# Kernel tuning notes

Measured on AMD Instinct MI355X. Metric: run time of the kernel, lower is better.

## Reference

```python
import jax, jax.numpy as jnp
import numpy as np

NEG_SLOPE = 0.2
EPS = 1e-16


def add_self_loops(edge_index, num_nodes):
    loops = jnp.arange(num_nodes, dtype=edge_index.dtype)
    loops = jnp.stack([loops, loops])  # [2, N]
    return jnp.concatenate([edge_index, loops], axis=1)


def gat_conv(x, edge_index, W, att_src, att_dst, bias, heads, out_c, concat):
    # x: [N, F_in]; edge_index: [2, E] (src row 0 -> dst row 1)
    N = x.shape[0]
    h = (x @ W).reshape(N, heads, out_c)            # [N, H, C]
    src, dst = edge_index[0], edge_index[1]
    a_src = (h * att_src).sum(-1)                    # [N, H]
    a_dst = (h * att_dst).sum(-1)                    # [N, H]
    e = a_src[src] + a_dst[dst]                      # [E, H]
    e = jnp.where(e > 0, e, NEG_SLOPE * e)           # leaky_relu
    # segment softmax over destination node
    m = jax.ops.segment_max(e, dst, num_segments=N)  # [N, H]
    ex = jnp.exp(e - m[dst])                         # [E, H]
    denom = jax.ops.segment_sum(ex, dst, num_segments=N)  # [N, H]
    alpha = ex / (denom[dst] + EPS)                  # [E, H]
    msg = alpha[:, :, None] * h[src]                 # [E, H, C]
    out = jax.ops.segment_sum(msg, dst, num_segments=N)   # [N, H, C]
    if concat:
        out = out.reshape(N, heads * out_c)
    else:
        out = out.mean(axis=1)
    return out + bias


def setup_inputs() -> dict:
    key = jax.random.key(0)
    ks = jax.random.split(key, 12)
    N, E, F_IN, HID, H1, OUT = 100000, 1600000, 512, 8, 8, 40
    x = jax.random.normal(ks[0], (N, F_IN), dtype=jnp.float32)
    edge_index = jax.random.randint(ks[1], (2, E), 0, N, dtype=jnp.int64)
    glorot = lambda k, shp: jax.random.normal(k, shp, jnp.float32) * jnp.sqrt(2.0 / (shp[0] + shp[-1]))
    W1 = glorot(ks[2], (F_IN, H1 * HID))
    att_src1 = glorot(ks[3], (H1, HID))
    att_dst1 = glorot(ks[4], (H1, HID))
    b1 = jnp.zeros((H1 * HID,), jnp.float32)
    W2 = glorot(ks[5], (H1 * HID, 1 * OUT))
    att_src2 = glorot(ks[6], (1, OUT))
    att_dst2 = glorot(ks[7], (1, OUT))
    b2 = jnp.zeros((OUT,), jnp.float32)
    return {"x": x, "edge_index": edge_index, "W1": W1, "att_src1": att_src1,
            "att_dst1": att_dst1, "b1": b1, "W2": W2, "att_src2": att_src2,
            "att_dst2": att_dst2, "b2": b2}


def reference(x, edge_index, W1, att_src1, att_dst1, b1, W2, att_src2, att_dst2, b2):
    N = x.shape[0]
    ei = add_self_loops(edge_index, N)
    h = gat_conv(x, ei, W1, att_src1, att_dst1, b1, heads=8, out_c=8, concat=True)
    h = jax.nn.relu(h)
    # dropout p=0.0 / eval mode -> identity
    out = gat_conv(h, ei, W2, att_src2, att_dst2, b2, heads=1, out_c=40, concat=False)
    return jax.nn.log_softmax(out, axis=1)
```

## Files before the change

### kernel.cpp

```cpp
#include <hip/hip_runtime.h>
#include <math.h>

#define NEG_SLOPE 0.2f
#define EPS_DEN 1e-16f

__device__ __forceinline__ float leaky(float v) { return v > 0.f ? v : NEG_SLOPE * v; }

typedef __attribute__((ext_vector_type(8))) short bf16x8;
typedef __attribute__((ext_vector_type(4))) float f32x4;

__device__ __forceinline__ unsigned bf16rne(float f) {
    unsigned u = __float_as_uint(f);
    return (u + 0x7FFFu + ((u >> 16) & 1u)) >> 16;
}
__device__ __forceinline__ unsigned pack2(float a, float b) {
    return bf16rne(a) | (bf16rne(b) << 16);
}
__device__ __forceinline__ float bfu(unsigned short u) {
    return __uint_as_float(((unsigned)u) << 16);
}

__global__ __launch_bounds__(256) void gemm1_mfma(
    const float* __restrict__ x, const float* __restrict__ W1,
    unsigned short* __restrict__ h1b, int N)
{
    __shared__ __align__(16) unsigned short As[128 * 40];
    __shared__ __align__(16) unsigned short Bs[64 * 40];

    const int t = threadIdx.x;
    const int w = t >> 6;
    const int lane = t & 63;
    const int m16 = lane & 15;
    const int quad = lane >> 4;
    const int rowBase = blockIdx.x * 128;

    f32x4 acc[2][4];
#pragma unroll
    for (int i = 0; i < 2; ++i)
#pragma unroll
        for (int j = 0; j < 4; ++j) acc[i][j] = (f32x4){0.f, 0.f, 0.f, 0.f};

    const float4* x4 = (const float4*)x;

#pragma unroll 1
    for (int chunk = 0; chunk < 16; ++chunk) {
        const int k0 = chunk * 32;
#pragma unroll
        for (int r = 0; r < 4; ++r) {
            int e = t + r * 256;
            int row = e >> 3;
            int kg = e & 7;
            int grow = rowBase + row;
            float4 v = make_float4(0.f, 0.f, 0.f, 0.f);
            if (grow < N) v = x4[(size_t)grow * 128 + (k0 >> 2) + kg];
            uint2 pk = make_uint2(pack2(v.x, v.y), pack2(v.z, v.w));
            *(uint2*)&As[row * 40 + kg * 4] = pk;
        }
        {
            int c = lane;
            int jb = w * 8;
            float f[8];
#pragma unroll
            for (int j = 0; j < 8; ++j) f[j] = W1[(size_t)(k0 + jb + j) * 64 + c];
            uint4 pk;
            pk.x = pack2(f[0], f[1]); pk.y = pack2(f[2], f[3]);
            pk.z = pack2(f[4], f[5]); pk.w = pack2(f[6], f[7]);
            *(uint4*)&Bs[c * 40 + jb] = pk;
        }
        __syncthreads();
        bf16x8 a0 = *(const bf16x8*)&As[(w * 32 + m16) * 40 + quad * 8];
        bf16x8 a1 = *(const bf16x8*)&As[(w * 32 + 16 + m16) * 40 + quad * 8];
#pragma unroll
        for (int j = 0; j < 4; ++j) {
            bf16x8 b = *(const bf16x8*)&Bs[(j * 16 + m16) * 40 + quad * 8];
            acc[0][j] = __builtin_amdgcn_mfma_f32_16x16x32_bf16(a0, b, acc[0][j], 0, 0, 0);
            acc[1][j] = __builtin_amdgcn_mfma_f32_16x16x32_bf16(a1, b, acc[1][j], 0, 0, 0);
        }
        __syncthreads();
    }

#pragma unroll
    for (int i = 0; i < 2; ++i)
#pragma unroll
        for (int reg = 0; reg < 4; ++reg) {
            int r = rowBase + w * 32 + i * 16 + quad * 4 + reg;
            if (r < N) {
#pragma unroll
                for (int j = 0; j < 4; ++j)
                    h1b[(size_t)r * 64 + j * 16 + m16] = (unsigned short)bf16rne(acc[i][j][reg]);
            }
        }
}

__global__ __launch_bounds__(256) void att1_kernel(
    const unsigned short* __restrict__ h1b, const float* __restrict__ att_src,
    const float* __restrict__ att_dst, float* __restrict__ a_src,
    float* __restrict__ a_dst, int N)
{
    int g = blockIdx.x * 256 + threadIdx.x;
    int row = g >> 3, h = g & 7;
    if (row >= N) return;
    uint4 pk = *(const uint4*)(h1b + (size_t)row * 64 + h * 8);
    float v[8];
    v[0] = __uint_as_float(pk.x << 16); v[1] = __uint_as_float(pk.x & 0xFFFF0000u);
    v[2] = __uint_as_float(pk.y << 16); v[3] = __uint_as_float(pk.y & 0xFFFF0000u);
    v[4] = __uint_as_float(pk.z << 16); v[5] = __uint_as_float(pk.z & 0xFFFF0000u);
    v[6] = __uint_as_float(pk.w << 16); v[7] = __uint_as_float(pk.w & 0xFFFF0000u);
    float ps = 0.f, pd = 0.f;
#pragma unroll
    for (int c = 0; c < 8; ++c) {
        ps += v[c] * att_src[h * 8 + c];
        pd += v[c] * att_dst[h * 8 + c];
    }
    a_src[(size_t)row * 8 + h] = ps;
    a_dst[(size_t)row * 8 + h] = pd;
}

__global__ __launch_bounds__(256) void deg_kernel(
    const int* __restrict__ ei, unsigned* __restrict__ deg, int E, int Etot)
{
    int idx = blockIdx.x * blockDim.x + threadIdx.x;
    if (idx >= Etot) return;
    int d = (idx < E) ? ei[E + idx] : (idx - E);
    atomicAdd(&deg[d], 1u);
}

__global__ __launch_bounds__(256) void scanA_kernel(
    const unsigned* __restrict__ deg, unsigned* __restrict__ loc,
    unsigned* __restrict__ bsum, int N)
{
    __shared__ unsigned sh[256];
    int i = blockIdx.x * 256 + threadIdx.x;
    unsigned v = (i < N) ? deg[i] : 0u;
    sh[threadIdx.x] = v;
    __syncthreads();
    for (int off = 1; off < 256; off <<= 1) {
        unsigned u = (threadIdx.x >= (unsigned)off) ? sh[threadIdx.x - off] : 0u;
        __syncthreads();
        sh[threadIdx.x] += u;
        __syncthreads();
    }
    if (i < N) loc[i] = sh[threadIdx.x] - v;
    if (threadIdx.x == 255) bsum[blockIdx.x] = sh[255];
}

__global__ __launch_bounds__(1024) void scanB_kernel(unsigned* __restrict__ bsum, int nb)
{
    __shared__ unsigned sh[1024];
    int t = threadIdx.x;
    unsigned carry = 0;
    for (int base = 0; base < nb; base += 1024) {
        int i = base + t;
        unsigned v = (i < nb) ? bsum[i] : 0u;
        sh[t] = v;
        __syncthreads();
        for (int off = 1; off < 1024; off <<= 1) {
            unsigned u = (t >= off) ? sh[t - off] : 0u;
            __syncthreads();
            sh[t] += u;
            __syncthreads();
        }
        unsigned incl = sh[t];
        unsigned tot  = sh[1023];
        __syncthreads();
        if (i < nb) bsum[i] = incl - v + carry;
        carry += tot;
        __syncthreads();
    }
}

__global__ __launch_bounds__(256) void scanC_kernel(
    const unsigned* __restrict__ loc, const unsigned* __restrict__ bsum,
    unsigned* __restrict__ rowstart, unsigned* __restrict__ cursor, int N, int Etot)
{
    int i = blockIdx.x * 256 + threadIdx.x;
    if (i >= N) return;
    unsigned r = loc[i] + bsum[blockIdx.x];
    rowstart[i] = r;
    cursor[i] = r;
    if (i == 0) rowstart[N] = (unsigned)Etot;
}

__global__ __launch_bounds__(256) void scatter_kernel(
    const int* __restrict__ ei, unsigned* __restrict__ cursor,
    int* __restrict__ csr_src, int E, int Etot)
{
    int idx = blockIdx.x * blockDim.x + threadIdx.x;
    if (idx >= Etot) return;
    int s, d;
    if (idx < E) { s = ei[idx]; d = ei[E + idx]; } else { s = d = idx - E; }
    unsigned pos = atomicAdd(&cursor[d], 1u);
    csr_src[pos] = s;
}

__global__ __launch_bounds__(256) void aggr1_kernel(
    const unsigned* __restrict__ rowstart, const int* __restrict__ csr_src,
    const float* __restrict__ a_src, const float* __restrict__ a_dst,
    const unsigned short* __restrict__ h1b, const float* __restrict__ b1,
    float* __restrict__ h2, int N)
{
    int g = blockIdx.x * 4 + (threadIdx.x >> 6);
    int lane = threadIdx.x & 63;
    if (g >= N) return;
    int h = lane >> 3;
    float ad = a_dst[(size_t)g * 8 + h];
    unsigned k0 = rowstart[g], k1 = rowstart[g + 1];
    float acc0 = 0.f, acc1 = 0.f, acc2 = 0.f, acc3 = 0.f;
    float dn0 = 0.f, dn1 = 0.f, dn2 = 0.f, dn3 = 0.f;
    unsigned k = k0;
    for (; k + 4 <= k1; k += 4) {
        int s0 = csr_src[k],     s1 = csr_src[k + 1];
        int s2 = csr_src[k + 2], s3 = csr_src[k + 3];
        float p0 = __expf(leaky(a_src[(size_t)s0 * 8 + h] + ad));
        float p1 = __expf(leaky(a_src[(size_t)s1 * 8 + h] + ad));
        float p2 = __expf(leaky(a_src[(size_t)s2 * 8 + h] + ad));
        float p3 = __expf(leaky(a_src[(size_t)s3 * 8 + h] + ad));
        acc0 += p0 * bfu(h1b[(size_t)s0 * 64 + lane]); dn0 += p0;
        acc1 += p1 * bfu(h1b[(size_t)s1 * 64 + lane]); dn1 += p1;
        acc2 += p2 * bfu(h1b[(size_t)s2 * 64 + lane]); dn2 += p2;
        acc3 += p3 * bfu(h1b[(size_t)s3 * 64 + lane]); dn3 += p3;
    }
    for (; k < k1; ++k) {
        int s0 = csr_src[k];
        float p0 = __expf(leaky(a_src[(size_t)s0 * 8 + h] + ad));
        acc0 += p0 * bfu(h1b[(size_t)s0 * 64 + lane]); dn0 += p0;
    }
    float den = (dn0 + dn1) + (dn2 + dn3);
    float acc = (acc0 + acc1) + (acc2 + acc3);
    float v = acc / (den + EPS_DEN) + b1[lane];
    h2[(size_t)g * 64 + lane] = v > 0.f ? v : 0.f;
}

__global__ __launch_bounds__(256) void gemm2_kernel(
    const float* __restrict__ h2, const float* __restrict__ W2,
    const float* __restrict__ att_src2, const float* __restrict__ att_dst2,
    unsigned short* __restrict__ h3b, float* __restrict__ a_src, float* __restrict__ a_dst, int N)
{
    __shared__ float Wl[64 * 40];
    int t = threadIdx.x;
    for (int i = t; i < 64 * 40; i += 256) Wl[i] = W2[i];
    __syncthreads();
    int lane = t & 63, wy = t >> 6;
    int row = blockIdx.x * 4 + wy;
    if (row >= N) return;
    float acc = 0.f;
    const float* hr = h2 + (size_t)row * 64;
    if (lane < 40) {
#pragma unroll 8
        for (int k = 0; k < 64; ++k) acc += hr[k] * Wl[k * 40 + lane];
        h3b[(size_t)row * 40 + lane] = (unsigned short)bf16rne(acc);
    }
    float ps = (lane < 40) ? acc * att_src2[lane] : 0.f;
    float pd = (lane < 40) ? acc * att_dst2[lane] : 0.f;
#pragma unroll
    for (int off = 32; off; off >>= 1) { ps += __shfl_down(ps, off); pd += __shfl_down(pd, off); }
    if (lane == 0) { a_src[row] = ps; a_dst[row] = pd; }
}

__global__ __launch_bounds__(256) void aggr2_kernel(
    const unsigned* __restrict__ rowstart, const int* __restrict__ csr_src,
    const float* __restrict__ a_src, const float* __restrict__ a_dst,
    const unsigned short* __restrict__ h3b, const float* __restrict__ b2,
    float* __restrict__ y, int N)
{
    int g = blockIdx.x * 4 + (threadIdx.x >> 6);
    int lane = threadIdx.x & 63;
    if (g >= N) return;
    float ad = a_dst[g];
    unsigned k0 = rowstart[g], k1 = rowstart[g + 1];
    float acc0 = 0.f, acc1 = 0.f, acc2 = 0.f, acc3 = 0.f;
    float dn0 = 0.f, dn1 = 0.f, dn2 = 0.f, dn3 = 0.f;
    unsigned k = k0;
    for (; k + 4 <= k1; k += 4) {
        int s0 = csr_src[k],     s1 = csr_src[k + 1];
        int s2 = csr_src[k + 2], s3 = csr_src[k + 3];
        float p0 = __expf(leaky(a_src[s0] + ad));
        float p1 = __expf(leaky(a_src[s1] + ad));
        float p2 = __expf(leaky(a_src[s2] + ad));
        float p3 = __expf(leaky(a_src[s3] + ad));
        float hv0 = (lane < 40) ? bfu(h3b[(size_t)s0 * 40 + lane]) : 0.f;
        float hv1 = (lane < 40) ? bfu(h3b[(size_t)s1 * 40 + lane]) : 0.f;
        float hv2 = (lane < 40) ? bfu(h3b[(size_t)s2 * 40 + lane]) : 0.f;
        float hv3 = (lane < 40) ? bfu(h3b[(size_t)s3 * 40 + lane]) : 0.f;
        acc0 += p0 * hv0; dn0 += p0;
        acc1 += p1 * hv1; dn1 += p1;
        acc2 += p2 * hv2; dn2 += p2;
        acc3 += p3 * hv3; dn3 += p3;
    }
    for (; k < k1; ++k) {
        int s0 = csr_src[k];
        float p0 = __expf(leaky(a_src[s0] + ad));
        float hv0 = (lane < 40) ? bfu(h3b[(size_t)s0 * 40 + lane]) : 0.f;
        acc0 += p0 * hv0; dn0 += p0;
    }
    float den = (dn0 + dn1) + (dn2 + dn3);
    float acc = (acc0 + acc1) + (acc2 + acc3);
    float v = (lane < 40) ? (acc / (den + EPS_DEN) + b2[lane]) : -INFINITY;
    float mx = v;
#pragma unroll
    for (int off = 32; off; off >>= 1) mx = fmaxf(mx, __shfl_down(mx, off));
    mx = __shfl(mx, 0);
    float ex = (lane < 40) ? expf(v - mx) : 0.f;
    float ss = ex;
#pragma unroll
    for (int off = 32; off; off >>= 1) ss += __shfl_down(ss, off);
    ss = __shfl(ss, 0);
    if (lane < 40) y[(size_t)g * 40 + lane] = v - mx - logf(ss);
}

extern "C" void kernel_launch(void* const* d_in, const int* in_sizes, int n_in,
                              void* d_out, int out_size, void* d_ws, size_t ws_size,
                              hipStream_t stream)
{
    const float* x        = (const float*)d_in[0];
    const int*   ei       = (const int*)d_in[1];
    const float* W1       = (const float*)d_in[2];
    const float* att_src1 = (const float*)d_in[3];
    const float* att_dst1 = (const float*)d_in[4];
    const float* b1       = (const float*)d_in[5];
    const float* W2       = (const float*)d_in[6];
    const float* att_src2 = (const float*)d_in[7];
    const float* att_dst2 = (const float*)d_in[8];
    const float* b2       = (const float*)d_in[9];
    float* y = (float*)d_out;

    int N = in_sizes[0] / 512;
    int E = in_sizes[1] / 2;
    int Etot = E + N;
    int nb = (N + 255) / 256;

    char* p = (char*)d_ws;
    unsigned short* h1b = (unsigned short*)p; p += (size_t)N * 64 * 2;
    float* a_src1a  = (float*)p;   p += (size_t)N * 8 * 4;
    float* a_dst1a  = (float*)p;   p += (size_t)N * 8 * 4;
    float* h2       = (float*)p;   p += (size_t)N * 64 * 4;
    unsigned short* h3b = (unsigned short*)p; p += (size_t)N * 40 * 2;
    float* a_src2a  = (float*)p;   p += (size_t)N * 4;
    float* a_dst2a  = (float*)p;   p += (size_t)N * 4;
    unsigned* deg   = (unsigned*)p; p += (size_t)N * 4;
    unsigned* loc   = (unsigned*)p; p += (size_t)N * 4;
    unsigned* bsum  = (unsigned*)p; p += (size_t)nb * 4;
    unsigned* rowstart = (unsigned*)p; p += (size_t)(N + 1) * 4;
    unsigned* cursor   = (unsigned*)p; p += (size_t)N * 4;
    int* csr_src    = (int*)p;     p += (size_t)Etot * 4;

    hipMemsetAsync(deg, 0, (size_t)N * 4, stream);

    gemm1_mfma<<<(N + 127) / 128, 256, 0, stream>>>(x, W1, h1b, N);
    att1_kernel<<<(N * 8 + 255) / 256, 256, 0, stream>>>(h1b, att_src1, att_dst1, a_src1a, a_dst1a, N);

    deg_kernel<<<(Etot + 255) / 256, 256, 0, stream>>>(ei, deg, E, Etot);
    scanA_kernel<<<nb, 256, 0, stream>>>(deg, loc, bsum, N);
    scanB_kernel<<<1, 1024, 0, stream>>>(bsum, nb);
    scanC_kernel<<<nb, 256, 0, stream>>>(loc, bsum, rowstart, cursor, N, Etot);
    scatter_kernel<<<(Etot + 255) / 256, 256, 0, stream>>>(ei, cursor, csr_src, E, Etot);

    aggr1_kernel<<<(N + 3) / 4, 256, 0, stream>>>(rowstart, csr_src, a_src1a, a_dst1a, h1b, b1, h2, N);

    gemm2_kernel<<<(N + 3) / 4, 256, 0, stream>>>(h2, W2, att_src2, att_dst2, h3b, a_src2a, a_dst2a, N);

    aggr2_kernel<<<(N + 3) / 4, 256, 0, stream>>>(rowstart, csr_src, a_src2a, a_dst2a, h3b, b2, y, N);
}
```

Measured before the change: 772.3 us.

## Slice CSR scatter by destination range, split layer-2 features, use hardware bf16 pack

```diff
diff --git a/kernel.cpp b/kernel.cpp
--- a/kernel.cpp
+++ b/kernel.cpp
@@ -14,7 +14,9 @@
     return (u + 0x7FFFu + ((u >> 16) & 1u)) >> 16;
 }
 __device__ __forceinline__ unsigned pack2(float a, float b) {
-    return bf16rne(a) | (bf16rne(b) << 16);
+    unsigned r;
+    asm("v_cvt_pk_bf16_f32 %0, %1, %2" : "=v"(r) : "v"(a), "v"(b));
+    return r;
 }
 __device__ __forceinline__ float bfu(unsigned short u) {
     return __uint_as_float(((unsigned)u) << 16);
@@ -183,12 +185,15 @@
 
 __global__ __launch_bounds__(256) void scatter_kernel(
     const int* __restrict__ ei, unsigned* __restrict__ cursor,
-    int* __restrict__ csr_src, int E, int Etot)
-{
-    int idx = blockIdx.x * blockDim.x + threadIdx.x;
+    int* __restrict__ csr_src, int E, int Etot, int sliceW)
+{
+    int slice = blockIdx.x & 7;
+    int idx = (blockIdx.x >> 3) * 256 + threadIdx.x;
     if (idx >= Etot) return;
-    int s, d;
-    if (idx < E) { s = ei[idx]; d = ei[E + idx]; } else { s = d = idx - E; }
+    int d = (idx < E) ? ei[E + idx] : (idx - E);
+    int lo = slice * sliceW;
+    if (d < lo || d >= lo + sliceW) return;
+    int s = (idx < E) ? ei[idx] : d;
     unsigned pos = atomicAdd(&cursor[d], 1u);
     csr_src[pos] = s;
 }
@@ -234,7 +239,8 @@
 __global__ __launch_bounds__(256) void gemm2_kernel(
     const float* __restrict__ h2, const float* __restrict__ W2,
     const float* __restrict__ att_src2, const float* __restrict__ att_dst2,
-    unsigned short* __restrict__ h3b, float* __restrict__ a_src, float* __restrict__ a_dst, int N)
+    unsigned short* __restrict__ h3b32, unsigned short* __restrict__ h3b8,
+    float* __restrict__ a_src, float* __restrict__ a_dst, int N)
 {
     __shared__ float Wl[64 * 40];
     int t = threadIdx.x;
@@ -248,7 +254,8 @@
     if (lane < 40) {
 #pragma unroll 8
         for (int k = 0; k < 64; ++k) acc += hr[k] * Wl[k * 40 + lane];
-        h3b[(size_t)row * 40 + lane] = (unsigned short)bf16rne(acc);
+        if (lane < 32) h3b32[(size_t)row * 32 + lane] = (unsigned short)bf16rne(acc);
+        else           h3b8[(size_t)row * 8 + (lane - 32)] = (unsigned short)bf16rne(acc);
     }
     float ps = (lane < 40) ? acc * att_src2[lane] : 0.f;
     float pd = (lane < 40) ? acc * att_dst2[lane] : 0.f;
@@ -260,12 +267,16 @@
 __global__ __launch_bounds__(256) void aggr2_kernel(
     const unsigned* __restrict__ rowstart, const int* __restrict__ csr_src,
     const float* __restrict__ a_src, const float* __restrict__ a_dst,
-    const unsigned short* __restrict__ h3b, const float* __restrict__ b2,
-    float* __restrict__ y, int N)
+    const unsigned short* __restrict__ h3b32, const unsigned short* __restrict__ h3b8,
+    const float* __restrict__ b2, float* __restrict__ y, int N)
 {
     int g = blockIdx.x * 4 + (threadIdx.x >> 6);
     int lane = threadIdx.x & 63;
     if (g >= N) return;
+    const bool valid = lane < 40;
+    const unsigned short* hsrc = (lane < 32) ? h3b32 : h3b8;
+    const int rowmul = (lane < 32) ? 32 : 8;
+    const int cidx   = (lane < 32) ? lane : (valid ? lane - 32 : 0);
     float ad = a_dst[g];
     unsigned k0 = rowstart[g], k1 = rowstart[g + 1];
     float acc0 = 0.f, acc1 = 0.f, acc2 = 0.f, acc3 = 0.f;
@@ -278,10 +289,11 @@
         float p1 = __expf(leaky(a_src[s1] + ad));
         float p2 = __expf(leaky(a_src[s2] + ad));
         float p3 = __expf(leaky(a_src[s3] + ad));
-        float hv0 = (lane < 40) ? bfu(h3b[(size_t)s0 * 40 + lane]) : 0.f;
-        float hv1 = (lane < 40) ? bfu(h3b[(size_t)s1 * 40 + lane]) : 0.f;
-        float hv2 = (lane < 40) ? bfu(h3b[(size_t)s2 * 40 + lane]) : 0.f;
-        float hv3 = (lane < 40) ? bfu(h3b[(size_t)s3 * 40 + lane]) : 0.f;
+        float hv0 = bfu(hsrc[(size_t)s0 * rowmul + cidx]);
+        float hv1 = bfu(hsrc[(size_t)s1 * rowmul + cidx]);
+        float hv2 = bfu(hsrc[(size_t)s2 * rowmul + cidx]);
+        float hv3 = bfu(hsrc[(size_t)s3 * rowmul + cidx]);
+        if (!valid) { hv0 = hv1 = hv2 = hv3 = 0.f; }
         acc0 += p0 * hv0; dn0 += p0;
         acc1 += p1 * hv1; dn1 += p1;
         acc2 += p2 * hv2; dn2 += p2;
@@ -290,22 +302,22 @@
     for (; k < k1; ++k) {
         int s0 = csr_src[k];
         float p0 = __expf(leaky(a_src[s0] + ad));
-        float hv0 = (lane < 40) ? bfu(h3b[(size_t)s0 * 40 + lane]) : 0.f;
+        float hv0 = valid ? bfu(hsrc[(size_t)s0 * rowmul + cidx]) : 0.f;
         acc0 += p0 * hv0; dn0 += p0;
     }
     float den = (dn0 + dn1) + (dn2 + dn3);
     float acc = (acc0 + acc1) + (acc2 + acc3);
-    float v = (lane < 40) ? (acc / (den + EPS_DEN) + b2[lane]) : -INFINITY;
+    float v = valid ? (acc / (den + EPS_DEN) + b2[lane]) : -INFINITY;
     float mx = v;
 #pragma unroll
     for (int off = 32; off; off >>= 1) mx = fmaxf(mx, __shfl_down(mx, off));
     mx = __shfl(mx, 0);
-    float ex = (lane < 40) ? expf(v - mx) : 0.f;
+    float ex = valid ? expf(v - mx) : 0.f;
     float ss = ex;
 #pragma unroll
     for (int off = 32; off; off >>= 1) ss += __shfl_down(ss, off);
     ss = __shfl(ss, 0);
-    if (lane < 40) y[(size_t)g * 40 + lane] = v - mx - logf(ss);
+    if (valid) y[(size_t)g * 40 + lane] = v - mx - logf(ss);
 }
 
 extern "C" void kernel_launch(void* const* d_in, const int* in_sizes, int n_in,
@@ -328,13 +340,15 @@
     int E = in_sizes[1] / 2;
     int Etot = E + N;
     int nb = (N + 255) / 256;
+    int sliceW = (N + 7) / 8;
 
     char* p = (char*)d_ws;
     unsigned short* h1b = (unsigned short*)p; p += (size_t)N * 64 * 2;
     float* a_src1a  = (float*)p;   p += (size_t)N * 8 * 4;
     float* a_dst1a  = (float*)p;   p += (size_t)N * 8 * 4;
     float* h2       = (float*)p;   p += (size_t)N * 64 * 4;
-    unsigned short* h3b = (unsigned short*)p; p += (size_t)N * 40 * 2;
+    unsigned short* h3b32 = (unsigned short*)p; p += (size_t)N * 32 * 2;
+    unsigned short* h3b8  = (unsigned short*)p; p += (size_t)N * 8 * 2;
     float* a_src2a  = (float*)p;   p += (size_t)N * 4;
     float* a_dst2a  = (float*)p;   p += (size_t)N * 4;
     unsigned* deg   = (unsigned*)p; p += (size_t)N * 4;
@@ -353,11 +367,11 @@
     scanA_kernel<<<nb, 256, 0, stream>>>(deg, loc, bsum, N);
     scanB_kernel<<<1, 1024, 0, stream>>>(bsum, nb);
     scanC_kernel<<<nb, 256, 0, stream>>>(loc, bsum, rowstart, cursor, N, Etot);
-    scatter_kernel<<<(Etot + 255) / 256, 256, 0, stream>>>(ei, cursor, csr_src, E, Etot);
+    scatter_kernel<<<8 * ((Etot + 255) / 256), 256, 0, stream>>>(ei, cursor, csr_src, E, Etot, sliceW);
 
     aggr1_kernel<<<(N + 3) / 4, 256, 0, stream>>>(rowstart, csr_src, a_src1a, a_dst1a, h1b, b1, h2, N);
 
-    gemm2_kernel<<<(N + 3) / 4, 256, 0, stream>>>(h2, W2, att_src2, att_dst2, h3b, a_src2a, a_dst2a, N);
-
-    aggr2_kernel<<<(N + 3) / 4, 256, 0, stream>>>(rowstart, csr_src, a_src2a, a_dst2a, h3b, b2, y, N);
-}
+    gemm2_kernel<<<(N + 3) / 4, 256, 0, stream>>>(h2, W2, att_src2, att_dst2, h3b32, h3b8, a_src2a, a_dst2a, N);
+
+    aggr2_kernel<<<(N + 3) / 4, 256, 0, stream>>>(rowstart, csr_src, a_src2a, a_dst2a, h3b32, h3b8, b2, y, N);
+}
```

After: 692.4 us. 1.12x faster.
